# Performance work log

Measured on AMD Instinct MI355X. Metric: run time of the kernel, lower is better.

## Reference

```python
import jax, jax.numpy as jnp
import numpy as np

EPS = 1e-4

def setup_inputs() -> dict:
    key = jax.random.key(0)
    ks = jax.random.split(key, 8)
    B, S, D, N = 4, 4096, 1024, 256
    return {
        "tokens": jax.random.normal(ks[0], (B, S, D), dtype=jnp.float32),
        "norm_w": jnp.ones((D,), dtype=jnp.float32),
        "W_in": jax.random.normal(ks[1], (N, D), dtype=jnp.float32) * (1.0 / np.sqrt(D)),
        "b_in": jax.random.normal(ks[2], (N,), dtype=jnp.float32) * 0.02,
        "W_out": jax.random.normal(ks[3], (D, N), dtype=jnp.float32) * (1.0 / np.sqrt(N)),
        "b_out": jax.random.normal(ks[4], (D,), dtype=jnp.float32) * 0.02,
        "W_skip": jax.random.normal(ks[5], (D, D), dtype=jnp.float32) * (1.0 / np.sqrt(D)),
        "b_skip": jax.random.normal(ks[6], (D,), dtype=jnp.float32) * 0.02,
        "log_decay": jnp.zeros((N,), dtype=jnp.float32),
    }

def reference(tokens, norm_w, W_in, b_in, W_out, b_out, W_skip, b_skip, log_decay):
    # RMSNorm (eps=1e-4), matching torch nn.RMSNorm
    ms = jnp.mean(tokens * tokens, axis=-1, keepdims=True)
    x = tokens * jax.lax.rsqrt(ms + EPS) * norm_w  # [B,S,D]

    decay = jax.nn.sigmoid(log_decay)  # [N]
    u = jnp.einsum("bsd,nd->bsn", x, W_in) + b_in  # [B,S,N] input projection, batched

    def step(state, u_t):  # state [B,N], u_t [B,N]
        state = decay * state + u_t
        return state, state

    B, S, _ = x.shape
    init = jnp.zeros((B, W_in.shape[0]), dtype=x.dtype)
    _, states = jax.lax.scan(step, init, jnp.swapaxes(u, 0, 1))  # [S,B,N]
    states = jnp.swapaxes(states, 0, 1)  # [B,S,N]

    y = jnp.einsum("bsn,dn->bsd", states, W_out) + b_out
    y = y + jnp.einsum("bsd,ed->bse", x, W_skip) + b_skip
    return tokens + y
```

## Files before the change

kernel.cpp:

```cpp
#include <hip/hip_runtime.h>

typedef __bf16 bf16_t;
typedef __bf16 bf16x4 __attribute__((ext_vector_type(4)));
typedef __bf16 bf16x8 __attribute__((ext_vector_type(8)));
typedef float  f32x4  __attribute__((ext_vector_type(4)));

#define ASYNC_COPY16(gp, lp)                                                     \
  __builtin_amdgcn_global_load_lds(                                              \
      (const __attribute__((address_space(1))) void*)(gp),                       \
      (__attribute__((address_space(3))) void*)(lp), 16, 0, 0)

__global__ __launch_bounds__(256) void k_prep(const float* __restrict__ tokens,
                                              const float* __restrict__ norm_w,
                                              bf16_t* __restrict__ x,
                                              const float* __restrict__ W_in,
                                              bf16_t* __restrict__ Wi,
                                              const float* __restrict__ W_out,
                                              bf16_t* __restrict__ Wo,
                                              const float* __restrict__ W_skip,
                                              bf16_t* __restrict__ Wsk) {
  const int bid = blockIdx.x;
  const int tid = threadIdx.x;
  if (bid < 1536) {
    const float* s;
    bf16_t* d;
    int i;
    if (bid < 256)      { s = W_in;   d = Wi;  i = bid * 256 + tid; }
    else if (bid < 512) { s = W_out;  d = Wo;  i = (bid - 256) * 256 + tid; }
    else                { s = W_skip; d = Wsk; i = (bid - 512) * 256 + tid; }
    float4 v = ((const float4*)s)[i];
    bf16x4 o;
    o[0] = (bf16_t)v.x; o[1] = (bf16_t)v.y; o[2] = (bf16_t)v.z; o[3] = (bf16_t)v.w;
    ((bf16x4*)d)[i] = o;
    return;
  }
  const int row = (bid - 1536) * 4 + (tid >> 6);
  const int lane = tid & 63;
  const size_t base = (size_t)row * 1024;
  const float4* tp = (const float4*)(tokens + base);
  float4 v[4];
  float ss = 0.0f;
#pragma unroll
  for (int i = 0; i < 4; ++i) {
    v[i] = tp[i * 64 + lane];
    ss += v[i].x * v[i].x + v[i].y * v[i].y + v[i].z * v[i].z + v[i].w * v[i].w;
  }
#pragma unroll
  for (int off = 32; off > 0; off >>= 1) ss += __shfl_xor(ss, off);
  const float scale = rsqrtf(ss * (1.0f / 1024.0f) + 1e-4f);
  bf16x4* xp = (bf16x4*)(x + base);
#pragma unroll
  for (int i = 0; i < 4; ++i) {
    float4 wv = ((const float4*)norm_w)[i * 64 + lane];
    bf16x4 o;
    o[0] = (bf16_t)(v[i].x * scale * wv.x);
    o[1] = (bf16_t)(v[i].y * scale * wv.y);
    o[2] = (bf16_t)(v[i].z * scale * wv.z);
    o[3] = (bf16_t)(v[i].w * scale * wv.w);
    xp[i * 64 + lane] = o;
  }
}

__global__ __launch_bounds__(256, 4) void k_gemm1(const bf16_t* __restrict__ A,
                                                  const bf16_t* __restrict__ Bw,
                                                  const float* __restrict__ bias,
                                                  bf16_t* __restrict__ C) {
  constexpr int K = 1024, Nc = 256;
  __shared__ __align__(16) bf16_t sA[64 * 64];
  __shared__ __align__(16) bf16_t sB[64 * 64];
  const int tid = threadIdx.x;
  const int lane = tid & 63;
  const int w = tid >> 6;
  const int wm = w >> 1, wn = w & 1;

  const int bid = blockIdx.x;
  const int swz = (bid & 7) * 128 + (bid >> 3);
  const int bm = swz >> 2;
  const int bn = swz & 3;

  const int st_row = tid >> 3;
  const int st_col = ((tid & 7) ^ ((tid >> 3) & 7)) * 8;
  const int lds_off = tid * 8;

  f32x4 acc[2][2] = {};

  for (int k0 = 0; k0 < K; k0 += 64) {
#pragma unroll
    for (int j = 0; j < 2; ++j)
      ASYNC_COPY16(A + (size_t)(bm * 64 + j * 32 + st_row) * K + k0 + st_col,
                   &sA[j * 2048 + lds_off]);
#pragma unroll
    for (int j = 0; j < 2; ++j)
      ASYNC_COPY16(Bw + (size_t)(bn * 64 + j * 32 + st_row) * K + k0 + st_col,
                   &sB[j * 2048 + lds_off]);
    __syncthreads();

#pragma unroll
    for (int kk = 0; kk < 2; ++kk) {
      const int slot = ((kk * 4 + (lane >> 4)) ^ (lane & 7)) * 8;
      bf16x8 af[2], bfr[2];
#pragma unroll
      for (int m = 0; m < 2; ++m)
        af[m] = *(const bf16x8*)&sA[(wm * 32 + m * 16 + (lane & 15)) * 64 + slot];
#pragma unroll
      for (int n = 0; n < 2; ++n)
        bfr[n] = *(const bf16x8*)&sB[(wn * 32 + n * 16 + (lane & 15)) * 64 + slot];
#pragma unroll
      for (int m = 0; m < 2; ++m)
#pragma unroll
        for (int n = 0; n < 2; ++n)
          acc[m][n] = __builtin_amdgcn_mfma_f32_16x16x32_bf16(af[m], bfr[n],
                                                              acc[m][n], 0, 0, 0);
    }
    __syncthreads();
  }

#pragma unroll
  for (int n = 0; n < 2; ++n) {
    const int col = bn * 64 + wn * 32 + n * 16 + (lane & 15);
    const float bv = bias[col];
#pragma unroll
    for (int m = 0; m < 2; ++m) {
      const int rbase = bm * 64 + wm * 32 + m * 16 + (lane >> 4) * 4;
#pragma unroll
      for (int j = 0; j < 4; ++j)
        C[(size_t)(rbase + j) * Nc + col] = (bf16_t)(acc[m][n][j] + bv);
    }
  }
}

__global__ __launch_bounds__(256) void k_scan(const bf16_t* __restrict__ u,
                                              const float* __restrict__ log_decay,
                                              bf16_t* __restrict__ states) {
  const int n = threadIdx.x;
  const int c = blockIdx.x;
  const int b = blockIdx.y;
  const float decay = 1.0f / (1.0f + __expf(-log_decay[n]));
  const bf16_t* up = u + (size_t)b * 4096 * 256 + n;
  bf16_t* sp = states + (size_t)b * 4096 * 256 + n;
  const int t0 = c * 64;
  const int tb = (c == 0) ? 0 : t0 - 64;
  const int te = t0 + 64;
  float state = 0.0f;
  for (int tblk = tb; tblk < te; tblk += 8) {
    float v[8];
#pragma unroll
    for (int q = 0; q < 8; ++q) v[q] = (float)up[(size_t)(tblk + q) * 256];
#pragma unroll
    for (int q = 0; q < 8; ++q) {
      state = fmaf(decay, state, v[q]);
      if (tblk + q >= t0) sp[(size_t)(tblk + q) * 256] = (bf16_t)state;
    }
  }
}

__global__ __launch_bounds__(256) void k_gemm2(const bf16_t* __restrict__ St,
                                               const bf16_t* __restrict__ X,
                                               const bf16_t* __restrict__ Wo,
                                               const bf16_t* __restrict__ Wsk,
                                               const float* __restrict__ tokens,
                                               const float* __restrict__ b_out,
                                               const float* __restrict__ b_skip,
                                               float* __restrict__ out) {
  __shared__ __align__(16) bf16_t sA[128 * 64];
  __shared__ __align__(16) bf16_t sB[128 * 64];
  const int tid = threadIdx.x;
  const int lane = tid & 63;
  const int w = tid >> 6;
  const int wm = w >> 1, wn = w & 1;

  const int bid = blockIdx.x;
  const int swz = (bid & 7) * 128 + (bid >> 3);
  const int bm = swz >> 3;
  const int bn = swz & 7;

  const int st_row = tid >> 3;
  const int st_col = ((tid & 7) ^ ((tid >> 3) & 7)) * 8;
  const int lds_off = tid * 8;

  f32x4 acc[4][4] = {};

  for (int kt = 0; kt < 20; ++kt) {
    const bf16_t* Ab;
    const bf16_t* Bb;
    int ld, kb;
    if (kt < 4) { Ab = St; Bb = Wo;  ld = 256;  kb = kt * 64; }
    else        { Ab = X;  Bb = Wsk; ld = 1024; kb = (kt - 4) * 64; }
#pragma unroll
    for (int it = 0; it < 4; ++it)
      ASYNC_COPY16(Ab + (size_t)(bm * 128 + it * 32 + st_row) * ld + kb + st_col,
                   &sA[it * 2048 + lds_off]);
#pragma unroll
    for (int it = 0; it < 4; ++it)
      ASYNC_COPY16(Bb + (size_t)(bn * 128 + it * 32 + st_row) * ld + kb + st_col,
                   &sB[it * 2048 + lds_off]);
    __syncthreads();

#pragma unroll
    for (int kk = 0; kk < 2; ++kk) {
      const int slot = ((kk * 4 + (lane >> 4)) ^ (lane & 7)) * 8;
      bf16x8 af[4], bfr[4];
#pragma unroll
      for (int m = 0; m < 4; ++m)
        af[m] = *(const bf16x8*)&sA[(wm * 64 + m * 16 + (lane & 15)) * 64 + slot];
#pragma unroll
      for (int n = 0; n < 4; ++n)
        bfr[n] = *(const bf16x8*)&sB[(wn * 64 + n * 16 + (lane & 15)) * 64 + slot];
#pragma unroll
      for (int m = 0; m < 4; ++m)
#pragma unroll
        for (int n = 0; n < 4; ++n)
          acc[m][n] = __builtin_amdgcn_mfma_f32_16x16x32_bf16(af[m], bfr[n],
                                                              acc[m][n], 0, 0, 0);
    }
    __syncthreads();
  }

#pragma unroll
  for (int n = 0; n < 4; ++n) {
    const int col = bn * 128 + wn * 64 + n * 16 + (lane & 15);
    const float bv = b_out[col] + b_skip[col];
#pragma unroll
    for (int m = 0; m < 4; ++m) {
      const int rbase = bm * 128 + wm * 64 + m * 16 + (lane >> 4) * 4;
#pragma unroll
      for (int j = 0; j < 4; ++j) {
        const size_t idx = (size_t)(rbase + j) * 1024 + col;
        out[idx] = acc[m][n][j] + tokens[idx] + bv;
      }
    }
  }
}

extern "C" void kernel_launch(void* const* d_in, const int* in_sizes, int n_in,
                              void* d_out, int out_size, void* d_ws, size_t ws_size,
                              hipStream_t stream) {
  const float* tokens  = (const float*)d_in[0];
  const float* norm_w  = (const float*)d_in[1];
  const float* W_in    = (const float*)d_in[2];
  const float* b_in    = (const float*)d_in[3];
  const float* W_out   = (const float*)d_in[4];
  const float* b_out   = (const float*)d_in[5];
  const float* W_skip  = (const float*)d_in[6];
  const float* b_skip  = (const float*)d_in[7];
  const float* log_dec = (const float*)d_in[8];
  float* out = (float*)d_out;

  char* w = (char*)d_ws;
  bf16_t* xb  = (bf16_t*)(w);
  bf16_t* u   = (bf16_t*)(w + 33554432ull);
  bf16_t* st  = (bf16_t*)(w + 41943040ull);
  bf16_t* Wi  = (bf16_t*)(w + 50331648ull);
  bf16_t* Wo  = (bf16_t*)(w + 50855936ull);
  bf16_t* Wsk = (bf16_t*)(w + 51380224ull);

  k_prep<<<dim3(5632), 256, 0, stream>>>(tokens, norm_w, xb, W_in, Wi,
                                         W_out, Wo, W_skip, Wsk);

  k_gemm1<<<dim3(1024), 256, 0, stream>>>(xb, Wi, b_in, u);

  k_scan<<<dim3(64, 4), 256, 0, stream>>>(u, log_dec, st);

  k_gemm2<<<dim3(1024), 256, 0, stream>>>(st, xb, Wo, Wsk, tokens, b_out,
                                          b_skip, out);
}
```

Baseline: 127.3 us.

## Fuse RMSNorm into input-projection GEMM with full-N row tiles

RMSNorm no longer runs in the prep kernel. It moves into a new fused kernel where each block normalizes 32 token rows, writes them to global memory as bf16, then computes the full 256-column projection for those rows. The GEMM tiling changes from 64x64 tiles over 1024 blocks to 32x256 tiles over 512 blocks, so each block reads its A rows once instead of four times. The cost is that the whole Wi K-slice is reloaded into shared memory by every block, there is less parallelism, and the GEMM re-reads from global memory the xb rows the block just wrote.

```diff
diff --git a/kernel.cpp b/kernel.cpp
--- a/kernel.cpp
+++ b/kernel.cpp
@@ -10,122 +10,107 @@
       (const __attribute__((address_space(1))) void*)(gp),                       \
       (__attribute__((address_space(3))) void*)(lp), 16, 0, 0)
 
-__global__ __launch_bounds__(256) void k_prep(const float* __restrict__ tokens,
-                                              const float* __restrict__ norm_w,
-                                              bf16_t* __restrict__ x,
-                                              const float* __restrict__ W_in,
-                                              bf16_t* __restrict__ Wi,
-                                              const float* __restrict__ W_out,
-                                              bf16_t* __restrict__ Wo,
-                                              const float* __restrict__ W_skip,
-                                              bf16_t* __restrict__ Wsk) {
+__global__ __launch_bounds__(256) void k_cvt(const float* __restrict__ W_in,
+                                             bf16_t* __restrict__ Wi,
+                                             const float* __restrict__ W_out,
+                                             bf16_t* __restrict__ Wo,
+                                             const float* __restrict__ W_skip,
+                                             bf16_t* __restrict__ Wsk) {
   const int bid = blockIdx.x;
   const int tid = threadIdx.x;
-  if (bid < 1536) {
-    const float* s;
-    bf16_t* d;
-    int i;
-    if (bid < 256)      { s = W_in;   d = Wi;  i = bid * 256 + tid; }
-    else if (bid < 512) { s = W_out;  d = Wo;  i = (bid - 256) * 256 + tid; }
-    else                { s = W_skip; d = Wsk; i = (bid - 512) * 256 + tid; }
-    float4 v = ((const float4*)s)[i];
-    bf16x4 o;
-    o[0] = (bf16_t)v.x; o[1] = (bf16_t)v.y; o[2] = (bf16_t)v.z; o[3] = (bf16_t)v.w;
-    ((bf16x4*)d)[i] = o;
-    return;
-  }
-  const int row = (bid - 1536) * 4 + (tid >> 6);
-  const int lane = tid & 63;
-  const size_t base = (size_t)row * 1024;
-  const float4* tp = (const float4*)(tokens + base);
-  float4 v[4];
-  float ss = 0.0f;
-#pragma unroll
-  for (int i = 0; i < 4; ++i) {
-    v[i] = tp[i * 64 + lane];
-    ss += v[i].x * v[i].x + v[i].y * v[i].y + v[i].z * v[i].z + v[i].w * v[i].w;
-  }
-#pragma unroll
-  for (int off = 32; off > 0; off >>= 1) ss += __shfl_xor(ss, off);
-  const float scale = rsqrtf(ss * (1.0f / 1024.0f) + 1e-4f);
-  bf16x4* xp = (bf16x4*)(x + base);
-#pragma unroll
-  for (int i = 0; i < 4; ++i) {
-    float4 wv = ((const float4*)norm_w)[i * 64 + lane];
-    bf16x4 o;
-    o[0] = (bf16_t)(v[i].x * scale * wv.x);
-    o[1] = (bf16_t)(v[i].y * scale * wv.y);
-    o[2] = (bf16_t)(v[i].z * scale * wv.z);
-    o[3] = (bf16_t)(v[i].w * scale * wv.w);
-    xp[i * 64 + lane] = o;
-  }
-}
-
-__global__ __launch_bounds__(256, 4) void k_gemm1(const bf16_t* __restrict__ A,
-                                                  const bf16_t* __restrict__ Bw,
+  const float* s;
+  bf16_t* d;
+  int i;
+  if (bid < 256)      { s = W_in;   d = Wi;  i = bid * 256 + tid; }
+  else if (bid < 512) { s = W_out;  d = Wo;  i = (bid - 256) * 256 + tid; }
+  else                { s = W_skip; d = Wsk; i = (bid - 512) * 256 + tid; }
+  float4 v = ((const float4*)s)[i];
+  bf16x4 o;
+  o[0] = (bf16_t)v.x; o[1] = (bf16_t)v.y; o[2] = (bf16_t)v.z; o[3] = (bf16_t)v.w;
+  ((bf16x4*)d)[i] = o;
+}
+
+__global__ __launch_bounds__(256, 2) void k_fused(const float* __restrict__ tokens,
+                                                  const float* __restrict__ norm_w,
+                                                  bf16_t* __restrict__ xb,
+                                                  const bf16_t* __restrict__ Wi,
                                                   const float* __restrict__ bias,
-                                                  bf16_t* __restrict__ C) {
-  constexpr int K = 1024, Nc = 256;
-  __shared__ __align__(16) bf16_t sA[64 * 64];
-  __shared__ __align__(16) bf16_t sB[64 * 64];
+                                                  bf16_t* __restrict__ u) {
+  __shared__ __align__(16) bf16_t sA[32 * 64];
+  __shared__ __align__(16) bf16_t sB[256 * 64];
   const int tid = threadIdx.x;
   const int lane = tid & 63;
   const int w = tid >> 6;
+  const int bm = blockIdx.x;
+
+  {
+    float4 wv[4];
+#pragma unroll
+    for (int i = 0; i < 4; ++i) wv[i] = ((const float4*)norm_w)[i * 64 + lane];
+    for (int r = 0; r < 8; ++r) {
+      const size_t base = ((size_t)bm * 32 + w * 8 + r) * 1024;
+      const float4* tp = (const float4*)(tokens + base);
+      float4 v[4];
+      float ss = 0.0f;
+#pragma unroll
+      for (int i = 0; i < 4; ++i) {
+        v[i] = tp[i * 64 + lane];
+        ss += v[i].x * v[i].x + v[i].y * v[i].y + v[i].z * v[i].z + v[i].w * v[i].w;
+      }
+#pragma unroll
+      for (int off = 32; off > 0; off >>= 1) ss += __shfl_xor(ss, off);
+      const float scale = rsqrtf(ss * (1.0f / 1024.0f) + 1e-4f);
+      bf16x4* xp = (bf16x4*)(xb + base);
+#pragma unroll
+      for (int i = 0; i < 4; ++i) {
+        bf16x4 o;
+        o[0] = (bf16_t)(v[i].x * scale * wv[i].x);
+        o[1] = (bf16_t)(v[i].y * scale * wv[i].y);
+        o[2] = (bf16_t)(v[i].z * scale * wv[i].z);
+        o[3] = (bf16_t)(v[i].w * scale * wv[i].w);
+        xp[i * 64 + lane] = o;
+      }
+    }
+  }
+  __syncthreads();
+
   const int wm = w >> 1, wn = w & 1;
-
-  const int bid = blockIdx.x;
-  const int swz = (bid & 7) * 128 + (bid >> 3);
-  const int bm = swz >> 2;
-  const int bn = swz & 3;
-
   const int st_row = tid >> 3;
   const int st_col = ((tid & 7) ^ ((tid >> 3) & 7)) * 8;
   const int lds_off = tid * 8;
 
-  f32x4 acc[2][2] = {};
-
-  for (int k0 = 0; k0 < K; k0 += 64) {
-#pragma unroll
-    for (int j = 0; j < 2; ++j)
-      ASYNC_COPY16(A + (size_t)(bm * 64 + j * 32 + st_row) * K + k0 + st_col,
-                   &sA[j * 2048 + lds_off]);
-#pragma unroll
-    for (int j = 0; j < 2; ++j)
-      ASYNC_COPY16(Bw + (size_t)(bn * 64 + j * 32 + st_row) * K + k0 + st_col,
-                   &sB[j * 2048 + lds_off]);
+  f32x4 acc[8] = {};
+
+  for (int k0 = 0; k0 < 1024; k0 += 64) {
+    ASYNC_COPY16(xb + ((size_t)bm * 32 + st_row) * 1024 + k0 + st_col,
+                 &sA[lds_off]);
+#pragma unroll
+    for (int it = 0; it < 8; ++it)
+      ASYNC_COPY16(Wi + (size_t)(it * 32 + st_row) * 1024 + k0 + st_col,
+                   &sB[it * 2048 + lds_off]);
     __syncthreads();
 
 #pragma unroll
     for (int kk = 0; kk < 2; ++kk) {
       const int slot = ((kk * 4 + (lane >> 4)) ^ (lane & 7)) * 8;
-      bf16x8 af[2], bfr[2];
-#pragma unroll
-      for (int m = 0; m < 2; ++m)
-        af[m] = *(const bf16x8*)&sA[(wm * 32 + m * 16 + (lane & 15)) * 64 + slot];
-#pragma unroll
-      for (int n = 0; n < 2; ++n)
-        bfr[n] = *(const bf16x8*)&sB[(wn * 32 + n * 16 + (lane & 15)) * 64 + slot];
-#pragma unroll
-      for (int m = 0; m < 2; ++m)
-#pragma unroll
-        for (int n = 0; n < 2; ++n)
-          acc[m][n] = __builtin_amdgcn_mfma_f32_16x16x32_bf16(af[m], bfr[n],
-                                                              acc[m][n], 0, 0, 0);
-    }
-    __syncthreads();
-  }
-
-#pragma unroll
-  for (int n = 0; n < 2; ++n) {
-    const int col = bn * 64 + wn * 32 + n * 16 + (lane & 15);
+      bf16x8 af = *(const bf16x8*)&sA[(wm * 16 + (lane & 15)) * 64 + slot];
+#pragma unroll
+      for (int n = 0; n < 8; ++n) {
+        bf16x8 bfr = *(const bf16x8*)&sB[(wn * 128 + n * 16 + (lane & 15)) * 64 + slot];
+        acc[n] = __builtin_amdgcn_mfma_f32_16x16x32_bf16(af, bfr, acc[n], 0, 0, 0);
+      }
+    }
+    __syncthreads();
+  }
+
+  const int row0 = bm * 32 + wm * 16 + (lane >> 4) * 4;
+#pragma unroll
+  for (int n = 0; n < 8; ++n) {
+    const int col = wn * 128 + n * 16 + (lane & 15);
     const float bv = bias[col];
 #pragma unroll
-    for (int m = 0; m < 2; ++m) {
-      const int rbase = bm * 64 + wm * 32 + m * 16 + (lane >> 4) * 4;
-#pragma unroll
-      for (int j = 0; j < 4; ++j)
-        C[(size_t)(rbase + j) * Nc + col] = (bf16_t)(acc[m][n][j] + bv);
-    }
+    for (int j = 0; j < 4; ++j)
+      u[(size_t)(row0 + j) * 256 + col] = (bf16_t)(acc[n][j] + bv);
   }
 }
 
@@ -254,10 +239,9 @@
   bf16_t* Wo  = (bf16_t*)(w + 50855936ull);
   bf16_t* Wsk = (bf16_t*)(w + 51380224ull);
 
-  k_prep<<<dim3(5632), 256, 0, stream>>>(tokens, norm_w, xb, W_in, Wi,
-                                         W_out, Wo, W_skip, Wsk);
-
-  k_gemm1<<<dim3(1024), 256, 0, stream>>>(xb, Wi, b_in, u);
+  k_cvt<<<dim3(1536), 256, 0, stream>>>(W_in, Wi, W_out, Wo, W_skip, Wsk);
+
+  k_fused<<<dim3(512), 256, 0, stream>>>(tokens, norm_w, xb, Wi, b_in, u);
 
   k_scan<<<dim3(64, 4), 256, 0, stream>>>(u, log_dec, st);
 
```

Measured after the change: 134.0 us. 1.05x slower.
